# Performance work log

Measured on AMD Instinct MI355X. Metric: run time of the kernel, lower is better.

The kernel has to match this reference:

```python
import jax, jax.numpy as jnp
import numpy as np

B, S, D = 8, 4096, 768
HEADS = 12
NEIGHBORS = 2
DILATION = 1
KERNEL = 1 + 2 * NEIGHBORS  # 5
DIM_HEAD = D // HEADS


def setup_inputs() -> dict:
    key = jax.random.key(0)
    ks = jax.random.split(key, 11)
    sc = 1.0 / np.sqrt(D)
    return {
        "x": jax.random.normal(ks[0], (B, S, D), dtype=jnp.float32),
        "Wq": jax.random.normal(ks[1], (D, D), dtype=jnp.float32) * sc,
        "bq": jax.random.normal(ks[2], (D,), dtype=jnp.float32) * 0.02,
        "Wk": jax.random.normal(ks[3], (D, D), dtype=jnp.float32) * sc,
        "bk": jax.random.normal(ks[4], (D,), dtype=jnp.float32) * 0.02,
        "Wv": jax.random.normal(ks[5], (D, D), dtype=jnp.float32) * sc,
        "bv": jax.random.normal(ks[6], (D,), dtype=jnp.float32) * 0.02,
        "Wo": jax.random.normal(ks[7], (D, D), dtype=jnp.float32) * sc,
        "bo": jax.random.normal(ks[8], (D,), dtype=jnp.float32) * 0.02,
        "gamma": jnp.ones((D,), dtype=jnp.float32),
        "beta": jnp.zeros((D,), dtype=jnp.float32),
    }


def _extract_seq_patches(x, kernel_size, dilation):
    # [B, S, D] -> [B, S, kernel_size, D] of dilated local windows, zero-padded.
    seq_len = x.shape[1]
    patch_size = kernel_size + (dilation - 1) * (kernel_size - 1)
    pad_r = (patch_size - 1) // 2
    pad_l = patch_size - pad_r - 1
    xp = jnp.pad(x, ((0, 0), (pad_l, pad_r), (0, 0)))
    # small fixed loop over kernel positions (kernel_size = 5)
    return jnp.stack([xp[:, i:i + seq_len] for i in range(0, patch_size, dilation)], axis=2)


def reference(x, Wq, bq, Wk, bk, Wv, bv, Wo, bo, gamma, beta):
    patches = _extract_seq_patches(x, KERNEL, DILATION)  # [B, S, K, D]
    q = x @ Wq + bq                                       # [B, S, D]
    k = patches @ Wk + bk                                 # [B, S, K, D]
    v = patches @ Wv + bv                                 # [B, S, K, D]
    # split heads
    q = q.reshape(B, S, HEADS, DIM_HEAD)
    k = k.reshape(B, S, KERNEL, HEADS, DIM_HEAD)
    v = v.reshape(B, S, KERNEL, HEADS, DIM_HEAD)
    scale = jnp.sqrt(jnp.asarray(DIM_HEAD, dtype=q.dtype))
    scores = jnp.einsum('bshd,bskhd->bshk', q, k) / scale  # [B, S, H, K]
    p = jax.nn.softmax(scores, axis=-1)
    att = jnp.einsum('bshk,bskhd->bshd', p, v)             # [B, S, H, dh]
    att = att.reshape(B, S, D)
    att = att @ Wo + bo
    y = att + x
    # LayerNorm over last dim
    mu = jnp.mean(y, axis=-1, keepdims=True)
    var = jnp.var(y, axis=-1, keepdims=True)
    y = (y - mu) / jnp.sqrt(var + 1e-5) * gamma + beta
    return y
```

## Files before the change

### kernel.cpp

```cpp
#include <hip/hip_runtime.h>

#define B_  8
#define S_  4096
#define D_  768
#define H_  12
#define M_  (B_ * S_)
#define NQKV_ 2304
#define NTILES 12

typedef unsigned short u16;
typedef __attribute__((ext_vector_type(4))) float  f32x4;
typedef __attribute__((ext_vector_type(8))) __bf16 bf16x8;
typedef __attribute__((ext_vector_type(4))) u16    u16x4;

#define GAS __attribute__((address_space(1)))
#define LAS __attribute__((address_space(3)))

__device__ __forceinline__ u16 f2bf(float f) {
    unsigned u = __float_as_uint(f);
    u += 0x7FFF + ((u >> 16) & 1);
    return (u16)(u >> 16);
}
__device__ __forceinline__ float bf2f(u16 h) {
    return __uint_as_float(((unsigned)h) << 16);
}

__device__ __forceinline__ void gload_lds16(const void* g, void* l) {
    __builtin_amdgcn_global_load_lds((const GAS void*)g, (LAS void*)l, 16, 0, 0);
}

__device__ __forceinline__ int xcd_swz(int bid, int nwg) {
    return (bid & 7) * (nwg >> 3) + (bid >> 3);
}

__global__ __launch_bounds__(256) void castx_kernel(const float* __restrict__ x,
                                                    u16* __restrict__ xb) {
    const int i = blockIdx.x * 256 + threadIdx.x;
    const float4 v = ((const float4*)x)[i];
    u16x4 o;
    o.x = f2bf(v.x); o.y = f2bf(v.y); o.z = f2bf(v.z); o.w = f2bf(v.w);
    ((u16x4*)xb)[i] = o;
}

__global__ __launch_bounds__(256) void wtrans_kernel(const float* __restrict__ Wq,
                                                     const float* __restrict__ Wk,
                                                     const float* __restrict__ Wv,
                                                     const float* __restrict__ Wo,
                                                     u16* __restrict__ Wb) {
    const float* W = (blockIdx.z == 0) ? Wq : (blockIdx.z == 1) ? Wk
                   : (blockIdx.z == 2) ? Wv : Wo;
    u16* O = Wb + (size_t)blockIdx.z * D_ * D_;
    __shared__ float tile[32][33];
    const int tx = threadIdx.x & 31, ty = threadIdx.x >> 5;
    const int k0 = blockIdx.y * 32, n0 = blockIdx.x * 32;
#pragma unroll
    for (int j = 0; j < 4; j++)
        tile[ty + j * 8][tx] = W[(size_t)(k0 + ty + j * 8) * D_ + n0 + tx];
    __syncthreads();
#pragma unroll
    for (int j = 0; j < 4; j++)
        O[(size_t)(n0 + ty + j * 8) * D_ + k0 + tx] = f2bf(tile[tx][ty + j * 8]);
}


#define MFMA16(AF, BF)                                                       \
    __builtin_amdgcn_s_setprio(1);                                           \
    _Pragma("unroll") for (int mi = 0; mi < 4; ++mi)                         \
        _Pragma("unroll") for (int ni = 0; ni < 4; ++ni)                     \
            acc[mi][ni] = __builtin_amdgcn_mfma_f32_16x16x32_bf16(           \
                AF[mi], BF[ni], acc[mi][ni], 0, 0, 0);                       \
    __builtin_amdgcn_s_setprio(0)

#define RD(p, imm) (*(const bf16x8*)((p) + (imm)))

template <int MODE>
__global__ __launch_bounds__(512, 4) void gemmf_kernel(
    const u16* __restrict__ A, const u16* __restrict__ Wb,
    const float* __restrict__ b0, const float* __restrict__ b1,
    const float* __restrict__ b2,
    u16* __restrict__ outb, const u16* __restrict__ xres) {
    extern __shared__ char lds[];

    const int t = threadIdx.x;
    const int w = t >> 6, l = t & 63;
    const int wm = w >> 2, wn = w & 3;

    const int NTN = (MODE == 0) ? 9 : 3;
    const int work = xcd_swz(blockIdx.x, gridDim.x);
    const int mt = work / NTN, nt = work % NTN;
    const int m0 = mt * 128;
    const int n0 = nt * 256;
    const int widx = (MODE == 0) ? (n0 / D_) : 3;
    const int n0w = n0 - ((MODE == 0) ? widx * D_ : 0);

    const int sc   = l & 3;
    const int srA  = w * 16 + (l >> 2);
    const int srB  = w * 32 + (l >> 2);
    const int fA   = (srA ^ (srA >> 2)) & 3;
    const int fB   = (srB ^ (srB >> 2)) & 3;
    const u16* AsrcB = A + (size_t)(m0 + srA) * D_ + (sc ^ fA) * 8;
    const u16* BsrcB = Wb + (size_t)widx * (D_ * D_)
                          + (size_t)(n0w + srB) * D_ + (sc ^ fB) * 8;
    char* const dstA = lds + w * 1024;
    char* const dstB = lds + 24576 + w * 2048;

    const int fr   = l & 15;
    const int slot = (l >> 4) ^ ((fr ^ (fr >> 2)) & 3);
    const char* aBase = lds + (wm * 64 + fr) * 64 + slot * 16;
    const char* bBase = lds + 24576 + (wn * 64 + fr) * 64 + slot * 16;

    f32x4 acc[4][4];
#pragma unroll
    for (int i = 0; i < 4; i++)
#pragma unroll
        for (int j = 0; j < 4; j++) acc[i][j] = (f32x4){0.f, 0.f, 0.f, 0.f};

    gload_lds16(AsrcB, dstA);
    gload_lds16(BsrcB, dstB);
    gload_lds16(BsrcB + 16 * D_, dstB + 1024);
    gload_lds16(AsrcB + 32, dstA + 8192);
    gload_lds16(BsrcB + 32, dstB + 16384);
    gload_lds16(BsrcB + 32 + 16 * D_, dstB + 16384 + 1024);
    __builtin_amdgcn_sched_barrier(0);
    asm volatile("s_waitcnt vmcnt(3)" ::: "memory");
    __builtin_amdgcn_s_barrier();
    __builtin_amdgcn_sched_barrier(0);

#pragma unroll
    for (int p = 0; p < 2 * NTILES; ++p) {
        const int rg = p % 3;
        const int sg = (p + 2) % 3;
        const int Xs = (p + 2) >> 1;
        const int sX = (Xs >= NTILES) ? 0 : Xs;
        const int soff = sX * 64 + (p & 1) * 32;

        bf16x8 Af[4], Bf[4];
#pragma unroll
        for (int i = 0; i < 4; ++i)
            Af[i] = RD(aBase, rg * 8192 + i * 1024);
#pragma unroll
        for (int n = 0; n < 4; ++n)
            Bf[n] = RD(bBase, rg * 16384 + n * 1024);

        gload_lds16(AsrcB + soff, dstA + sg * 8192);
        gload_lds16(BsrcB + soff, dstB + sg * 16384);
        gload_lds16(BsrcB + soff + 16 * D_, dstB + sg * 16384 + 1024);

        __builtin_amdgcn_sched_barrier(0);
        asm volatile("s_waitcnt vmcnt(3)" ::: "memory");
        __builtin_amdgcn_s_barrier();
        asm volatile("s_waitcnt lgkmcnt(0)" ::: "memory");
        __builtin_amdgcn_sched_barrier(0);

        MFMA16(Af, Bf);

        __builtin_amdgcn_sched_barrier(0);
        __builtin_amdgcn_s_barrier();
        __builtin_amdgcn_sched_barrier(0);
    }
    asm volatile("s_waitcnt vmcnt(0)" ::: "memory");

    const int crow0 = m0 + wm * 64 + ((l >> 4) << 2);
    const int ccol0 = n0 + wn * 64 + fr;
    if (MODE == 0) {
        const float* bias = (widx == 0) ? b0 : (widx == 1) ? b1 : b2;
        const int bcol0 = ccol0 - widx * D_;
#pragma unroll
        for (int mi = 0; mi < 4; ++mi)
#pragma unroll
            for (int ni = 0; ni < 4; ++ni) {
                const float bv = bias[bcol0 + ni * 16];
#pragma unroll
                for (int r = 0; r < 4; ++r)
                    outb[(size_t)(crow0 + mi * 16 + r) * NQKV_ + ccol0 + ni * 16] =
                        f2bf(acc[mi][ni][r] + bv);
            }
    } else {
#pragma unroll
        for (int mi = 0; mi < 4; ++mi)
#pragma unroll
            for (int ni = 0; ni < 4; ++ni) {
                const int col = ccol0 + ni * 16;
                const float bv = b0[col];
#pragma unroll
                for (int r = 0; r < 4; ++r) {
                    const size_t idx = (size_t)(crow0 + mi * 16 + r) * D_ + col;
                    outb[idx] = f2bf(acc[mi][ni][r] + bv + bf2f(xres[idx]));
                }
            }
    }
}

__global__ __launch_bounds__(256) void attn_kernel(const u16* __restrict__ QKV,
                                                   const float* __restrict__ bk,
                                                   const float* __restrict__ bv,
                                                   u16* __restrict__ att) {
    const int gw = xcd_swz(blockIdx.x, gridDim.x) * 4 + (threadIdx.x >> 6);
    const int l  = threadIdx.x & 63;
    const int hq = gw % 3;
    const int m  = gw / 3;
    const int s  = m & (S_ - 1);
    const int col = hq * 256 + l * 4;
    const u16* base = QKV + (size_t)m * NQKV_;

    const u16x4 qv = *(const u16x4*)(base + col);
    float qf[4];
#pragma unroll
    for (int j = 0; j < 4; j++) qf[j] = bf2f(qv[j]);

    float sc[5];
#pragma unroll
    for (int i = 0; i < 5; i++) {
        const int sp = s + i - 2;
        float p;
        if (sp >= 0 && sp < S_) {
            const u16x4 kv = *(const u16x4*)(base + (i - 2) * NQKV_ + D_ + col);
            p = qf[0] * bf2f(kv[0]) + qf[1] * bf2f(kv[1])
              + qf[2] * bf2f(kv[2]) + qf[3] * bf2f(kv[3]);
        } else {
            const float4 kb = *(const float4*)(bk + col);
            p = qf[0] * kb.x + qf[1] * kb.y + qf[2] * kb.z + qf[3] * kb.w;
        }
#pragma unroll
        for (int off = 1; off < 16; off <<= 1) p += __shfl_xor(p, off, 64);
        sc[i] = p * 0.125f;
    }
    float mx = sc[0];
#pragma unroll
    for (int i = 1; i < 5; i++) mx = fmaxf(mx, sc[i]);
    float e[5], sum = 0.f;
#pragma unroll
    for (int i = 0; i < 5; i++) { e[i] = __expf(sc[i] - mx); sum += e[i]; }
    const float inv = 1.f / sum;

    float o[4] = {0.f, 0.f, 0.f, 0.f};
#pragma unroll
    for (int i = 0; i < 5; i++) {
        const float wgt = e[i] * inv;
        const int sp = s + i - 2;
        if (sp >= 0 && sp < S_) {
            const u16x4 vv = *(const u16x4*)(base + (i - 2) * NQKV_ + 2 * D_ + col);
#pragma unroll
            for (int j = 0; j < 4; j++) o[j] += wgt * bf2f(vv[j]);
        } else {
            const float4 vb = *(const float4*)(bv + col);
            o[0] += wgt * vb.x; o[1] += wgt * vb.y;
            o[2] += wgt * vb.z; o[3] += wgt * vb.w;
        }
    }
    u16x4 ov;
#pragma unroll
    for (int j = 0; j < 4; j++) ov[j] = f2bf(o[j]);
    *(u16x4*)(att + (size_t)m * D_ + col) = ov;
}

__global__ __launch_bounds__(256) void ln_kernel(const u16* __restrict__ Yb,
                                                 const float* __restrict__ gamma,
                                                 const float* __restrict__ beta,
                                                 float* __restrict__ out) {
    const int row = blockIdx.x;
    const u16* r = Yb + (size_t)row * D_;
    const int t = threadIdx.x;
    const float v0 = bf2f(r[t]), v1 = bf2f(r[t + 256]), v2 = bf2f(r[t + 512]);
    float s  = v0 + v1 + v2;
    float s2 = v0 * v0 + v1 * v1 + v2 * v2;
#pragma unroll
    for (int off = 32; off > 0; off >>= 1) {
        s  += __shfl_xor(s,  off, 64);
        s2 += __shfl_xor(s2, off, 64);
    }
    __shared__ float red[8];
    const int w = t >> 6, l = t & 63;
    if (l == 0) { red[w] = s; red[4 + w] = s2; }
    __syncthreads();
    s  = red[0] + red[1] + red[2] + red[3];
    s2 = red[4] + red[5] + red[6] + red[7];
    const float mu  = s * (1.f / 768.f);
    const float var = s2 * (1.f / 768.f) - mu * mu;
    const float inv = rsqrtf(var + 1e-5f);
    float* o = out + (size_t)row * D_;
    o[t]       = (v0 - mu) * inv * gamma[t]       + beta[t];
    o[t + 256] = (v1 - mu) * inv * gamma[t + 256] + beta[t + 256];
    o[t + 512] = (v2 - mu) * inv * gamma[t + 512] + beta[t + 512];
}

extern "C" void kernel_launch(void* const* d_in, const int* in_sizes, int n_in,
                              void* d_out, int out_size, void* d_ws, size_t ws_size,
                              hipStream_t stream) {
    const float* x     = (const float*)d_in[0];
    const float* Wq    = (const float*)d_in[1];
    const float* bq    = (const float*)d_in[2];
    const float* Wk    = (const float*)d_in[3];
    const float* bk    = (const float*)d_in[4];
    const float* Wv    = (const float*)d_in[5];
    const float* bv    = (const float*)d_in[6];
    const float* Wo    = (const float*)d_in[7];
    const float* bo    = (const float*)d_in[8];
    const float* gamma = (const float*)d_in[9];
    const float* beta  = (const float*)d_in[10];

    char* ws = (char*)d_ws;
    u16*   Wb  = (u16*)ws;
    u16*   xb  = (u16*)(ws + 4718592);
    u16*   QKV = (u16*)(ws + 4718592 + 50331648);
    u16*   yb  = QKV;
    u16*   att = (u16*)d_out;

    (void)hipFuncSetAttribute(reinterpret_cast<const void*>(&gemmf_kernel<0>),
                              hipFuncAttributeMaxDynamicSharedMemorySize, 73728);
    (void)hipFuncSetAttribute(reinterpret_cast<const void*>(&gemmf_kernel<1>),
                              hipFuncAttributeMaxDynamicSharedMemorySize, 73728);

    castx_kernel<<<(M_ * D_) / (256 * 4), 256, 0, stream>>>(x, xb);
    wtrans_kernel<<<dim3(24, 24, 4), 256, 0, stream>>>(Wq, Wk, Wv, Wo, Wb);
    gemmf_kernel<0><<<(M_ / 128) * 9, 512, 73728, stream>>>(xb, Wb, bq, bk, bv,
                                                            QKV, nullptr);
    attn_kernel<<<(M_ * 3) / 4, 256, 0, stream>>>(QKV, bk, bv, att);
    gemmf_kernel<1><<<(M_ / 128) * 3, 512, 73728, stream>>>(att, Wb, bo, nullptr, nullptr,
                                                            yb, xb);
    ln_kernel<<<M_, 256, 0, stream>>>(yb, gamma, beta, (float*)d_out);
}
```

Baseline: 306.3 us.

## Switch GEMMs to 128x128 tiles with double-buffered 64-wide K stages

```diff
diff --git a/kernel.cpp b/kernel.cpp
--- a/kernel.cpp
+++ b/kernel.cpp
@@ -63,10 +63,10 @@
 }
 
 
-#define MFMA16(AF, BF)                                                       \
+#define MFMA8(AF, BF)                                                        \
     __builtin_amdgcn_s_setprio(1);                                           \
     _Pragma("unroll") for (int mi = 0; mi < 4; ++mi)                         \
-        _Pragma("unroll") for (int ni = 0; ni < 4; ++ni)                     \
+        _Pragma("unroll") for (int ni = 0; ni < 2; ++ni)                     \
             acc[mi][ni] = __builtin_amdgcn_mfma_f32_16x16x32_bf16(           \
                 AF[mi], BF[ni], acc[mi][ni], 0, 0, 0);                       \
     __builtin_amdgcn_s_setprio(0)
@@ -74,7 +74,7 @@
 #define RD(p, imm) (*(const bf16x8*)((p) + (imm)))
 
 template <int MODE>
-__global__ __launch_bounds__(512, 4) void gemmf_kernel(
+__global__ __launch_bounds__(512, 4) void gemm2_kernel(
     const u16* __restrict__ A, const u16* __restrict__ Wb,
     const float* __restrict__ b0, const float* __restrict__ b1,
     const float* __restrict__ b2,
@@ -85,90 +85,76 @@
     const int w = t >> 6, l = t & 63;
     const int wm = w >> 2, wn = w & 3;
 
-    const int NTN = (MODE == 0) ? 9 : 3;
+    const int NTN = (MODE == 0) ? 18 : 6;
     const int work = xcd_swz(blockIdx.x, gridDim.x);
     const int mt = work / NTN, nt = work % NTN;
     const int m0 = mt * 128;
-    const int n0 = nt * 256;
-    const int widx = (MODE == 0) ? (n0 / D_) : 3;
-    const int n0w = n0 - ((MODE == 0) ? widx * D_ : 0);
-
-    const int sc   = l & 3;
-    const int srA  = w * 16 + (l >> 2);
-    const int srB  = w * 32 + (l >> 2);
-    const int fA   = (srA ^ (srA >> 2)) & 3;
-    const int fB   = (srB ^ (srB >> 2)) & 3;
-    const u16* AsrcB = A + (size_t)(m0 + srA) * D_ + (sc ^ fA) * 8;
-    const u16* BsrcB = Wb + (size_t)widx * (D_ * D_)
-                          + (size_t)(n0w + srB) * D_ + (sc ^ fB) * 8;
-    char* const dstA = lds + w * 1024;
-    char* const dstB = lds + 24576 + w * 2048;
-
-    const int fr   = l & 15;
-    const int slot = (l >> 4) ^ ((fr ^ (fr >> 2)) & 3);
-    const char* aBase = lds + (wm * 64 + fr) * 64 + slot * 16;
-    const char* bBase = lds + 24576 + (wn * 64 + fr) * 64 + slot * 16;
-
-    f32x4 acc[4][4];
+    const int col0 = nt * 128;
+    const int widx = (MODE == 0) ? (nt / 6) : 3;
+    const int n0w  = (MODE == 0) ? (nt % 6) * 128 : col0;
+
+    const int sr = w * 16 + (l >> 3);
+    const int sc = l & 7;
+    const int schunk = sc ^ (sr & 7);
+    const u16* Asrc = A + (size_t)(m0 + sr) * D_ + schunk * 8;
+    const u16* Bsrc = Wb + (size_t)widx * (D_ * D_)
+                         + (size_t)(n0w + sr) * D_ + schunk * 8;
+    char* const dstA = lds + w * 2048;
+    char* const dstB = lds + 16384 + w * 2048;
+
+    const int ck0 = (((l >> 4) ^ (l & 7)) << 4);
+    const int ck1 = ((((l >> 4) + 4) ^ (l & 7)) << 4);
+    const char* aB = lds + (wm * 64 + (l & 15)) * 128;
+    const char* bB = lds + 16384 + (wn * 32 + (l & 15)) * 128;
+
+    f32x4 acc[4][2];
 #pragma unroll
     for (int i = 0; i < 4; i++)
 #pragma unroll
-        for (int j = 0; j < 4; j++) acc[i][j] = (f32x4){0.f, 0.f, 0.f, 0.f};
-
-    gload_lds16(AsrcB, dstA);
-    gload_lds16(BsrcB, dstB);
-    gload_lds16(BsrcB + 16 * D_, dstB + 1024);
-    gload_lds16(AsrcB + 32, dstA + 8192);
-    gload_lds16(BsrcB + 32, dstB + 16384);
-    gload_lds16(BsrcB + 32 + 16 * D_, dstB + 16384 + 1024);
-    __builtin_amdgcn_sched_barrier(0);
-    asm volatile("s_waitcnt vmcnt(3)" ::: "memory");
-    __builtin_amdgcn_s_barrier();
-    __builtin_amdgcn_sched_barrier(0);
-
-#pragma unroll
-    for (int p = 0; p < 2 * NTILES; ++p) {
-        const int rg = p % 3;
-        const int sg = (p + 2) % 3;
-        const int Xs = (p + 2) >> 1;
-        const int sX = (Xs >= NTILES) ? 0 : Xs;
-        const int soff = sX * 64 + (p & 1) * 32;
-
-        bf16x8 Af[4], Bf[4];
-#pragma unroll
-        for (int i = 0; i < 4; ++i)
-            Af[i] = RD(aBase, rg * 8192 + i * 1024);
-#pragma unroll
-        for (int n = 0; n < 4; ++n)
-            Bf[n] = RD(bBase, rg * 16384 + n * 1024);
-
-        gload_lds16(AsrcB + soff, dstA + sg * 8192);
-        gload_lds16(BsrcB + soff, dstB + sg * 16384);
-        gload_lds16(BsrcB + soff + 16 * D_, dstB + sg * 16384 + 1024);
-
-        __builtin_amdgcn_sched_barrier(0);
-        asm volatile("s_waitcnt vmcnt(3)" ::: "memory");
-        __builtin_amdgcn_s_barrier();
-        asm volatile("s_waitcnt lgkmcnt(0)" ::: "memory");
-        __builtin_amdgcn_sched_barrier(0);
-
-        MFMA16(Af, Bf);
-
-        __builtin_amdgcn_sched_barrier(0);
-        __builtin_amdgcn_s_barrier();
-        __builtin_amdgcn_sched_barrier(0);
-    }
-    asm volatile("s_waitcnt vmcnt(0)" ::: "memory");
+        for (int j = 0; j < 2; j++) acc[i][j] = (f32x4){0.f, 0.f, 0.f, 0.f};
+
+    auto STAGE = [&](int tk, int b) {
+        const int ko = tk * 64;
+        char* da = dstA + b * 32768;
+        char* db = dstB + b * 32768;
+        gload_lds16(Asrc + ko, da);
+        gload_lds16(Asrc + ko + 8 * D_, da + 1024);
+        gload_lds16(Bsrc + ko, db);
+        gload_lds16(Bsrc + ko + 8 * D_, db + 1024);
+    };
+
+    STAGE(0, 0);
+    __syncthreads();
+
+#pragma unroll
+    for (int X = 0; X < NTILES; ++X) {
+        const int cb = (X & 1) * 32768;
+        if (X + 1 < NTILES) STAGE(X + 1, (X & 1) ^ 1);
+
+        bf16x8 af[4], bf[2];
+#pragma unroll
+        for (int mi = 0; mi < 4; ++mi) af[mi] = RD(aB, cb + mi * 2048 + ck0);
+#pragma unroll
+        for (int ni = 0; ni < 2; ++ni) bf[ni] = RD(bB, cb + ni * 2048 + ck0);
+        MFMA8(af, bf);
+#pragma unroll
+        for (int mi = 0; mi < 4; ++mi) af[mi] = RD(aB, cb + mi * 2048 + ck1);
+#pragma unroll
+        for (int ni = 0; ni < 2; ++ni) bf[ni] = RD(bB, cb + ni * 2048 + ck1);
+        MFMA8(af, bf);
+
+        __syncthreads();
+    }
 
     const int crow0 = m0 + wm * 64 + ((l >> 4) << 2);
-    const int ccol0 = n0 + wn * 64 + fr;
+    const int ccol0 = col0 + wn * 32 + (l & 15);
     if (MODE == 0) {
         const float* bias = (widx == 0) ? b0 : (widx == 1) ? b1 : b2;
         const int bcol0 = ccol0 - widx * D_;
 #pragma unroll
         for (int mi = 0; mi < 4; ++mi)
 #pragma unroll
-            for (int ni = 0; ni < 4; ++ni) {
+            for (int ni = 0; ni < 2; ++ni) {
                 const float bv = bias[bcol0 + ni * 16];
 #pragma unroll
                 for (int r = 0; r < 4; ++r)
@@ -179,7 +165,7 @@
 #pragma unroll
         for (int mi = 0; mi < 4; ++mi)
 #pragma unroll
-            for (int ni = 0; ni < 4; ++ni) {
+            for (int ni = 0; ni < 2; ++ni) {
                 const int col = ccol0 + ni * 16;
                 const float bv = b0[col];
 #pragma unroll
@@ -306,17 +292,17 @@
     u16*   yb  = QKV;
     u16*   att = (u16*)d_out;
 
-    (void)hipFuncSetAttribute(reinterpret_cast<const void*>(&gemmf_kernel<0>),
-                              hipFuncAttributeMaxDynamicSharedMemorySize, 73728);
-    (void)hipFuncSetAttribute(reinterpret_cast<const void*>(&gemmf_kernel<1>),
-                              hipFuncAttributeMaxDynamicSharedMemorySize, 73728);
+    (void)hipFuncSetAttribute(reinterpret_cast<const void*>(&gemm2_kernel<0>),
+                              hipFuncAttributeMaxDynamicSharedMemorySize, 65536);
+    (void)hipFuncSetAttribute(reinterpret_cast<const void*>(&gemm2_kernel<1>),
+                              hipFuncAttributeMaxDynamicSharedMemorySize, 65536);
 
     castx_kernel<<<(M_ * D_) / (256 * 4), 256, 0, stream>>>(x, xb);
     wtrans_kernel<<<dim3(24, 24, 4), 256, 0, stream>>>(Wq, Wk, Wv, Wo, Wb);
-    gemmf_kernel<0><<<(M_ / 128) * 9, 512, 73728, stream>>>(xb, Wb, bq, bk, bv,
-                                                            QKV, nullptr);
+    gemm2_kernel<0><<<(M_ / 128) * 18, 512, 65536, stream>>>(xb, Wb, bq, bk, bv,
+                                                             QKV, nullptr);
     attn_kernel<<<(M_ * 3) / 4, 256, 0, stream>>>(QKV, bk, bv, att);
-    gemmf_kernel<1><<<(M_ / 128) * 3, 512, 73728, stream>>>(att, Wb, bo, nullptr, nullptr,
+    gemm2_kernel<1><<<(M_ / 128) * 6, 512, 65536, stream>>>(att, Wb, bo, nullptr, nullptr,
                                                             yb, xb);
     ln_kernel<<<M_, 256, 0, stream>>>(yb, gamma, beta, (float*)d_out);
 }
```

Result: faster. 294.4 us (-3.9%).
